# Optimization experiments

Hardware: AMD Instinct MI355X
Metric: run time of the kernel (lower is better)

## Reference

```python
import jax, jax.numpy as jnp
import numpy as np

N = 16384
F = 256
RATIO = 0.5
K_KEEP = int(RATIO * N)  # 8192 nodes kept


def setup_inputs() -> dict:
    key = jax.random.key(0)
    k1, k2, k3 = jax.random.split(key, 3)
    X = jax.random.normal(k1, (N, F), dtype=jnp.float32)
    # binary-ish dense adjacency
    A = (jax.random.uniform(k2, (N, N), dtype=jnp.float32) < 0.01).astype(jnp.float32)
    p = jax.random.normal(k3, (F, 1), dtype=jnp.float32)
    return {"X": X, "A": A, "p": p}


def reference(X, A, p):
    # y = X p / ||p||  (scores), shape [N, 1]
    p_hat = p / jnp.sqrt(jnp.sum(p * p))
    y = X @ p_hat
    # global top-k (single-graph mode: I == zeros), indices sorted ascending
    _, idx = jax.lax.top_k(y[:, 0], K_KEEP)
    idx = jnp.sort(idx)
    # gated features, then gather kept nodes
    features = X * jnp.tanh(y)
    X_pooled = jnp.take(features, idx, axis=0)          # [K, F]
    # adjacency submatrix A[idx, idx]
    A_pooled = jnp.take(jnp.take(A, idx, axis=0), idx, axis=1)  # [K, K]
    return X_pooled, A_pooled
```

## Files before the change

kernel.cpp:

```cpp
#include <hip/hip_runtime.h>
#include <math.h>

#define N 16384
#define F 256
#define K_KEEP 8192
#define JCH 512
#define IPT 4
#define QS 4096
#define APOOL_BLOCKS (K_KEEP * 4)

typedef float f32x4 __attribute__((ext_vector_type(4)));

__global__ __launch_bounds__(256) void score_kernel(const float* __restrict__ X,
                                                    const float* __restrict__ p,
                                                    double* __restrict__ y,
                                                    unsigned long long* __restrict__ key) {
    const int wave = threadIdx.x >> 6;
    const int lane = threadIdx.x & 63;
    const int row  = blockIdx.x * 4 + wave;

    const float4 pv = *reinterpret_cast<const float4*>(p + lane * 4);
    const float4 xv = *reinterpret_cast<const float4*>(X + (size_t)row * F + lane * 4);

    double pp = (double)pv.x * pv.x + (double)pv.y * pv.y +
                (double)pv.z * pv.z + (double)pv.w * pv.w;
    double xp = (double)xv.x * pv.x + (double)xv.y * pv.y +
                (double)xv.z * pv.z + (double)xv.w * pv.w;

    #pragma unroll
    for (int off = 32; off >= 1; off >>= 1) {
        pp += __shfl_down(pp, off, 64);
        xp += __shfl_down(xp, off, 64);
    }
    if (lane == 0) {
        const double yy = xp / sqrt(pp);
        y[row] = yy;
        const long long b = __double_as_longlong(yy);
        key[row] = (unsigned long long)b ^
                   ((b < 0) ? 0xFFFFFFFFFFFFFFFFULL : 0x8000000000000000ULL);
    }
}

__global__ __launch_bounds__(256) void rank_kernel(const unsigned long long* __restrict__ key,
                                                   unsigned short* __restrict__ rankp) {
    __shared__ ulonglong2 kch2[JCH / 2];
    const int t     = threadIdx.x;
    const int jc    = blockIdx.y;
    const int jbase = jc * JCH;
    kch2[t] = *reinterpret_cast<const ulonglong2*>(key + jbase + 2 * t);
    __syncthreads();

    const int ibase = blockIdx.x * (256 * IPT) + t;
    const unsigned long long k0 = key[ibase];
    const unsigned long long k1 = key[ibase + 256];
    const unsigned long long k2 = key[ibase + 512];
    const unsigned long long k3 = key[ibase + 768];
    int c0 = 0, c1 = 0, c2 = 0, c3 = 0;
    #pragma unroll 8
    for (int jj = 0; jj < JCH / 2; ++jj) {
        const ulonglong2 kk = kch2[jj];
        c0 += (int)(kk.x > k0) + (int)(kk.y > k0);
        c1 += (int)(kk.x > k1) + (int)(kk.y > k1);
        c2 += (int)(kk.x > k2) + (int)(kk.y > k2);
        c3 += (int)(kk.x > k3) + (int)(kk.y > k3);
    }
    rankp[jc * N + ibase      ] = (unsigned short)c0;
    rankp[jc * N + ibase + 256] = (unsigned short)c1;
    rankp[jc * N + ibase + 512] = (unsigned short)c2;
    rankp[jc * N + ibase + 768] = (unsigned short)c3;
}

__global__ __launch_bounds__(256) void flags_kernel(const unsigned short* __restrict__ rankp,
                                                    unsigned long long* __restrict__ flagbits) {
    const int i = blockIdx.x * 256 + threadIdx.x;
    int r = 0;
    #pragma unroll
    for (int jc = 0; jc < N / JCH; ++jc) r += (int)rankp[jc * N + i];
    const bool kept = (r < K_KEEP);
    const unsigned long long m = __ballot(kept);
    if ((threadIdx.x & 63) == 0) flagbits[i >> 6] = m;
}

__global__ __launch_bounds__(256) void emit_kernel(const unsigned long long* __restrict__ flagbits,
                                                   int* __restrict__ idx,
                                                   unsigned short* __restrict__ srcq,
                                                   int* __restrict__ wexcl) {
    __shared__ int sc[256];
    const int t = threadIdx.x;
    const unsigned long long m = flagbits[t];
    const int c = __popcll(m);
    sc[t] = c;
    __syncthreads();
    for (int off = 1; off < 256; off <<= 1) {
        const int v = (t >= off) ? sc[t - off] : 0;
        __syncthreads();
        sc[t] += v;
        __syncthreads();
    }
    const int excl = sc[t] - c;
    wexcl[t] = excl;

    int base = excl;
    unsigned long long mm = m;
    const int col = t * 64;
    while (mm) {
        const int b = __ffsll((long long)mm) - 1;
        mm &= (mm - 1);
        const int i = col + b;
        idx[base]  = i;
        srcq[base] = (unsigned short)(i & (QS - 1));
        ++base;
    }
}

__global__ __launch_bounds__(256) void pool_kernel(const float* __restrict__ A,
                                                   const float* __restrict__ X,
                                                   const double* __restrict__ y,
                                                   const int* __restrict__ idx,
                                                   const unsigned short* __restrict__ srcq,
                                                   const int* __restrict__ wexcl,
                                                   float* __restrict__ outX,
                                                   float* __restrict__ outA) {
    const int t = threadIdx.x;

    if (blockIdx.x >= APOOL_BLOCKS) {
        const int k    = (blockIdx.x - APOOL_BLOCKS) * 4 + (t >> 6);
        const int lane = t & 63;
        const int src  = idx[k];
        const float tf = tanhf((float)y[src]);
        const float4 xv = *reinterpret_cast<const float4*>(X + (size_t)src * F + lane * 4);
        float4 o = {xv.x * tf, xv.y * tf, xv.z * tf, xv.w * tf};
        *reinterpret_cast<float4*>(outX + (size_t)k * F + lane * 4) = o;
        return;
    }

    __shared__ float buf[QS];
    const int row  = blockIdx.x >> 2;
    const int h    = blockIdx.x & 3;
    const int ridx = idx[row];
    const int kb   = wexcl[h * 64];
    const int ke   = (h < 3) ? wexcl[h * 64 + 64] : K_KEEP;

    const f32x4* __restrict__ a4 =
        reinterpret_cast<const f32x4*>(A + (size_t)ridx * N + h * QS);
    f32x4* __restrict__ b4 = reinterpret_cast<f32x4*>(buf);
    #pragma unroll
    for (int s = 0; s < 4; ++s) b4[s * 256 + t] = __builtin_nontemporal_load(a4 + s * 256 + t);
    __syncthreads();

    float* __restrict__ orow = outA + (size_t)row * K_KEEP;
    const int k4b = (kb + 3) & ~3;
    const int k4e = ke & ~3;
    if (t < (k4b - kb)) orow[kb + t] = buf[srcq[kb + t]];
    if (t < (ke - k4e)) orow[k4e + t] = buf[srcq[k4e + t]];
    for (int k4 = k4b + 4 * t; k4 < k4e; k4 += 1024) {
        const ushort4 s4 = *reinterpret_cast<const ushort4*>(srcq + k4);
        f32x4 v = {buf[s4.x], buf[s4.y], buf[s4.z], buf[s4.w]};
        __builtin_nontemporal_store(v, reinterpret_cast<f32x4*>(orow + k4));
    }
}

extern "C" void kernel_launch(void* const* d_in, const int* in_sizes, int n_in,
                              void* d_out, int out_size, void* d_ws, size_t ws_size,
                              hipStream_t stream) {
    const float* X = (const float*)d_in[0];
    const float* A = (const float*)d_in[1];
    const float* p = (const float*)d_in[2];

    float* out  = (float*)d_out;
    float* outX = out;
    float* outA = out + (size_t)K_KEEP * F;

    char* ws = (char*)d_ws;
    double*             y        = (double*)ws;
    unsigned long long* key      = (unsigned long long*)(ws + 131072);
    unsigned short*     rankp    = (unsigned short*)(ws + 262144);
    unsigned long long* flagbits = (unsigned long long*)(ws + 1310720);
    int*                wexcl    = (int*)(ws + 1312768);
    int*                idx      = (int*)(ws + 1313792);
    unsigned short*     srcq     = (unsigned short*)(ws + 1346560);

    score_kernel<<<N / 4, 256, 0, stream>>>(X, p, y, key);
    rank_kernel<<<dim3(N / (256 * IPT), N / JCH), 256, 0, stream>>>(key, rankp);
    flags_kernel<<<N / 256, 256, 0, stream>>>(rankp, flagbits);
    emit_kernel<<<1, 256, 0, stream>>>(flagbits, idx, srcq, wexcl);
    pool_kernel<<<APOOL_BLOCKS + K_KEEP / 4, 256, 0, stream>>>(A, X, y, idx, srcq, wexcl,
                                                               outX, outA);
}
```

Before: 178.6 us.

## Parallelize index emission across blocks and load A rows directly into LDS

Emission of kept indices moves from a single block, where each thread serially walks a 64-bit mask, to 64 blocks. Each block computes its global offset from per-block counts that the flags kernel now writes, then uses popcount prefix sums so every kept element is written in parallel. The pool kernel stages A row slices with global_load_lds (direct global-to-LDS DMA) instead of loading through registers and then storing to shared memory. Each block now re-sums up to 63 block counts, and the direct LDS load drops the nontemporal hint on A reads.

```diff
diff --git a/kernel.cpp b/kernel.cpp
--- a/kernel.cpp
+++ b/kernel.cpp
@@ -10,6 +10,8 @@
 #define APOOL_BLOCKS (K_KEEP * 4)
 
 typedef float f32x4 __attribute__((ext_vector_type(4)));
+typedef __attribute__((address_space(3))) char lds_char;
+typedef const __attribute__((address_space(1))) char glb_char;
 
 __global__ __launch_bounds__(256) void score_kernel(const float* __restrict__ X,
                                                     const float* __restrict__ p,
@@ -71,45 +73,57 @@
 }
 
 __global__ __launch_bounds__(256) void flags_kernel(const unsigned short* __restrict__ rankp,
-                                                    unsigned long long* __restrict__ flagbits) {
-    const int i = blockIdx.x * 256 + threadIdx.x;
+                                                    unsigned long long* __restrict__ flagbits,
+                                                    int* __restrict__ blkcnt) {
+    __shared__ int wc[4];
+    const int b = blockIdx.x;
+    const int i = b * 256 + threadIdx.x;
     int r = 0;
     #pragma unroll
     for (int jc = 0; jc < N / JCH; ++jc) r += (int)rankp[jc * N + i];
     const bool kept = (r < K_KEEP);
     const unsigned long long m = __ballot(kept);
-    if ((threadIdx.x & 63) == 0) flagbits[i >> 6] = m;
-}
-
-__global__ __launch_bounds__(256) void emit_kernel(const unsigned long long* __restrict__ flagbits,
+    const int lane = threadIdx.x & 63;
+    const int wave = threadIdx.x >> 6;
+    if (lane == 0) { flagbits[i >> 6] = m; wc[wave] = __popcll(m); }
+    __syncthreads();
+    if (threadIdx.x == 0) blkcnt[b] = wc[0] + wc[1] + wc[2] + wc[3];
+}
+
+__global__ __launch_bounds__(256) void emit_kernel(const int* __restrict__ blkcnt,
+                                                   const unsigned long long* __restrict__ flagbits,
                                                    int* __restrict__ idx,
                                                    unsigned short* __restrict__ srcq,
                                                    int* __restrict__ wexcl) {
-    __shared__ int sc[256];
+    __shared__ int bc[64];
+    __shared__ int woff[4];
     const int t = threadIdx.x;
-    const unsigned long long m = flagbits[t];
-    const int c = __popcll(m);
-    sc[t] = c;
-    __syncthreads();
-    for (int off = 1; off < 256; off <<= 1) {
-        const int v = (t >= off) ? sc[t - off] : 0;
-        __syncthreads();
-        sc[t] += v;
-        __syncthreads();
-    }
-    const int excl = sc[t] - c;
-    wexcl[t] = excl;
-
-    int base = excl;
-    unsigned long long mm = m;
-    const int col = t * 64;
-    while (mm) {
-        const int b = __ffsll((long long)mm) - 1;
-        mm &= (mm - 1);
-        const int i = col + b;
-        idx[base]  = i;
-        srcq[base] = (unsigned short)(i & (QS - 1));
-        ++base;
+    const int b = blockIdx.x;
+    if (t < 64) bc[t] = blkcnt[t];
+    __syncthreads();
+
+    int goff = 0;
+    for (int j = 0; j < b; ++j) goff += bc[j];
+
+    if (t < 4) {
+        int s = goff;
+        for (int q = 0; q < t; ++q) s += __popcll(flagbits[4 * b + q]);
+        wexcl[4 * b + t] = s;
+    }
+
+    const int i = b * 256 + t;
+    const unsigned long long m = flagbits[i >> 6];
+    const int lane = t & 63;
+    const int wave = t >> 6;
+    const bool kept = (m >> lane) & 1ull;
+    if (lane == 0) woff[wave] = __popcll(m);
+    __syncthreads();
+    int wbase = 0;
+    for (int w = 0; w < wave; ++w) wbase += woff[w];
+    const int pos = goff + wbase + __popcll(m & ((1ull << lane) - 1ull));
+    if (kept) {
+        idx[pos]  = i;
+        srcq[pos] = (unsigned short)(i & (QS - 1));
     }
 }
 
@@ -137,15 +151,20 @@
     __shared__ float buf[QS];
     const int row  = blockIdx.x >> 2;
     const int h    = blockIdx.x & 3;
+    const int wv   = t >> 6;
     const int ridx = idx[row];
     const int kb   = wexcl[h * 64];
     const int ke   = (h < 3) ? wexcl[h * 64 + 64] : K_KEEP;
 
-    const f32x4* __restrict__ a4 =
-        reinterpret_cast<const f32x4*>(A + (size_t)ridx * N + h * QS);
-    f32x4* __restrict__ b4 = reinterpret_cast<f32x4*>(buf);
+    const glb_char* gsrc = (const glb_char*)(A + (size_t)ridx * N + h * QS);
+    lds_char* lbase = (lds_char*)buf + (size_t)wv * 1024;
     #pragma unroll
-    for (int s = 0; s < 4; ++s) b4[s * 256 + t] = __builtin_nontemporal_load(a4 + s * 256 + t);
+    for (int q = 0; q < 4; ++q) {
+        __builtin_amdgcn_global_load_lds(
+            (const __attribute__((address_space(1))) unsigned int*)(gsrc + (size_t)(q * 256 + t) * 16),
+            (__attribute__((address_space(3))) unsigned int*)(lbase + (size_t)q * 4096),
+            16, 0, 0);
+    }
     __syncthreads();
 
     float* __restrict__ orow = outA + (size_t)row * K_KEEP;
@@ -179,11 +198,12 @@
     int*                wexcl    = (int*)(ws + 1312768);
     int*                idx      = (int*)(ws + 1313792);
     unsigned short*     srcq     = (unsigned short*)(ws + 1346560);
+    int*                blkcnt   = (int*)(ws + 1362944);
 
     score_kernel<<<N / 4, 256, 0, stream>>>(X, p, y, key);
     rank_kernel<<<dim3(N / (256 * IPT), N / JCH), 256, 0, stream>>>(key, rankp);
-    flags_kernel<<<N / 256, 256, 0, stream>>>(rankp, flagbits);
-    emit_kernel<<<1, 256, 0, stream>>>(flagbits, idx, srcq, wexcl);
+    flags_kernel<<<N / 256, 256, 0, stream>>>(rankp, flagbits, blkcnt);
+    emit_kernel<<<N / 256, 256, 0, stream>>>(blkcnt, flagbits, idx, srcq, wexcl);
     pool_kernel<<<APOOL_BLOCKS + K_KEEP / 4, 256, 0, stream>>>(A, X, y, idx, srcq, wexcl,
                                                                outX, outA);
 }
```

Result: slower. 187.8 us (+5.1%).

## Replace all-pairs rank counting with single-block radix select for top-k threshold

Applied to the files above, without the earlier changes.

Replaces the O(N^2) pairwise rank kernel and its partial-rank buffer with a single-block three-level radix histogram select that finds the K-th largest key, followed by a small candidate sort. Flags are then computed by comparing each key against that threshold. This removes about 268M comparisons and the rank-partials traffic. In exchange, the selection runs serially in one workgroup with shared-memory atomics. It also assumes unique keys and at most 256 candidates after 36 bits of prefix.

```diff
diff --git a/kernel.cpp b/kernel.cpp
--- a/kernel.cpp
+++ b/kernel.cpp
@@ -4,8 +4,6 @@
 #define N 16384
 #define F 256
 #define K_KEEP 8192
-#define JCH 512
-#define IPT 4
 #define QS 4096
 #define APOOL_BLOCKS (K_KEEP * 4)
 
@@ -41,42 +39,85 @@
     }
 }
 
-__global__ __launch_bounds__(256) void rank_kernel(const unsigned long long* __restrict__ key,
-                                                   unsigned short* __restrict__ rankp) {
-    __shared__ ulonglong2 kch2[JCH / 2];
-    const int t     = threadIdx.x;
-    const int jc    = blockIdx.y;
-    const int jbase = jc * JCH;
-    kch2[t] = *reinterpret_cast<const ulonglong2*>(key + jbase + 2 * t);
-    __syncthreads();
-
-    const int ibase = blockIdx.x * (256 * IPT) + t;
-    const unsigned long long k0 = key[ibase];
-    const unsigned long long k1 = key[ibase + 256];
-    const unsigned long long k2 = key[ibase + 512];
-    const unsigned long long k3 = key[ibase + 768];
-    int c0 = 0, c1 = 0, c2 = 0, c3 = 0;
-    #pragma unroll 8
-    for (int jj = 0; jj < JCH / 2; ++jj) {
-        const ulonglong2 kk = kch2[jj];
-        c0 += (int)(kk.x > k0) + (int)(kk.y > k0);
-        c1 += (int)(kk.x > k1) + (int)(kk.y > k1);
-        c2 += (int)(kk.x > k2) + (int)(kk.y > k2);
-        c3 += (int)(kk.x > k3) + (int)(kk.y > k3);
-    }
-    rankp[jc * N + ibase      ] = (unsigned short)c0;
-    rankp[jc * N + ibase + 256] = (unsigned short)c1;
-    rankp[jc * N + ibase + 512] = (unsigned short)c2;
-    rankp[jc * N + ibase + 768] = (unsigned short)c3;
-}
-
-__global__ __launch_bounds__(256) void flags_kernel(const unsigned short* __restrict__ rankp,
+__global__ __launch_bounds__(256) void select_kernel(const unsigned long long* __restrict__ key,
+                                                     unsigned long long* __restrict__ thr_out) {
+    __shared__ int hist[4096];
+    __shared__ int part[256];
+    __shared__ int bres[2];
+    __shared__ unsigned long long cand[256];
+    __shared__ int ccnt;
+    const int t = threadIdx.x;
+
+    int rank = K_KEEP - 1;
+    unsigned long long pval = 0, pmask = 0;
+
+    for (int lvl = 0; lvl < 3; ++lvl) {
+        const int shift = 52 - lvl * 12;
+        #pragma unroll
+        for (int q = 0; q < 16; ++q) hist[q * 256 + t] = 0;
+        __syncthreads();
+
+        for (int i = t; i < N; i += 256) {
+            const unsigned long long k = key[i];
+            if ((k & pmask) == pval)
+                atomicAdd(&hist[(int)((k >> shift) & 0xFFF)], 1);
+        }
+        __syncthreads();
+
+        int ps = 0;
+        #pragma unroll
+        for (int q = 0; q < 16; ++q) ps += hist[t * 16 + q];
+        part[t] = ps;
+        __syncthreads();
+        for (int off = 1; off < 256; off <<= 1) {
+            const int v = (t >= off) ? part[t - off] : 0;
+            __syncthreads();
+            part[t] += v;
+            __syncthreads();
+        }
+        const int total = part[255];
+        int acc = total - part[t];
+        int fb = -1, fr = 0;
+        #pragma unroll
+        for (int q = 15; q >= 0; --q) {
+            const int b = t * 16 + q;
+            const int h = hist[b];
+            if (fb < 0 && acc <= rank && acc + h > rank) { fb = b; fr = rank - acc; }
+            acc += h;
+        }
+        if (fb >= 0) { bres[0] = fb; bres[1] = fr; }
+        __syncthreads();
+        const int b = bres[0];
+        rank = bres[1];
+        pval |= ((unsigned long long)b) << shift;
+        pmask |= (0xFFFULL << shift);
+        __syncthreads();
+    }
+
+    if (t == 0) ccnt = 0;
+    __syncthreads();
+    for (int i = t; i < N; i += 256) {
+        const unsigned long long k = key[i];
+        if ((k & pmask) == pval) {
+            const int pos = atomicAdd(&ccnt, 1);
+            if (pos < 256) cand[pos] = k;
+        }
+    }
+    __syncthreads();
+    const int c = (ccnt < 256) ? ccnt : 256;
+    if (t < c) {
+        const unsigned long long kk = cand[t];
+        int cnt = 0;
+        for (int j = 0; j < c; ++j) cnt += (int)(cand[j] > kk);
+        if (cnt == rank) *thr_out = kk;
+    }
+}
+
+__global__ __launch_bounds__(256) void flags_kernel(const unsigned long long* __restrict__ key,
+                                                    const unsigned long long* __restrict__ thr,
                                                     unsigned long long* __restrict__ flagbits) {
     const int i = blockIdx.x * 256 + threadIdx.x;
-    int r = 0;
-    #pragma unroll
-    for (int jc = 0; jc < N / JCH; ++jc) r += (int)rankp[jc * N + i];
-    const bool kept = (r < K_KEEP);
+    const bool kept = key[i] >= *thr;
     const unsigned long long m = __ballot(kept);
     if ((threadIdx.x & 63) == 0) flagbits[i >> 6] = m;
 }
@@ -174,15 +215,15 @@
     char* ws = (char*)d_ws;
     double*             y        = (double*)ws;
     unsigned long long* key      = (unsigned long long*)(ws + 131072);
-    unsigned short*     rankp    = (unsigned short*)(ws + 262144);
-    unsigned long long* flagbits = (unsigned long long*)(ws + 1310720);
-    int*                wexcl    = (int*)(ws + 1312768);
-    int*                idx      = (int*)(ws + 1313792);
-    unsigned short*     srcq     = (unsigned short*)(ws + 1346560);
+    unsigned long long* flagbits = (unsigned long long*)(ws + 262144);
+    int*                wexcl    = (int*)(ws + 264192);
+    int*                idx      = (int*)(ws + 265216);
+    unsigned short*     srcq     = (unsigned short*)(ws + 297984);
+    unsigned long long* thr      = (unsigned long long*)(ws + 314368);
 
     score_kernel<<<N / 4, 256, 0, stream>>>(X, p, y, key);
-    rank_kernel<<<dim3(N / (256 * IPT), N / JCH), 256, 0, stream>>>(key, rankp);
-    flags_kernel<<<N / 256, 256, 0, stream>>>(rankp, flagbits);
+    select_kernel<<<1, 256, 0, stream>>>(key, thr);
+    flags_kernel<<<N / 256, 256, 0, stream>>>(key, thr, flagbits);
     emit_kernel<<<1, 256, 0, stream>>>(flagbits, idx, srcq, wexcl);
     pool_kernel<<<APOOL_BLOCKS + K_KEEP / 4, 256, 0, stream>>>(A, X, y, idx, srcq, wexcl,
                                                                outX, outA);
```

Result: slower. 212.0 us (+18.7%).
